# Kernel optimization log

Measured on AMD Instinct MI355X. Metric: run time of the kernel, lower is better.

## Reference

```python
import jax, jax.numpy as jnp
import numpy as np
import math


def setup_inputs() -> dict:
    key = jax.random.key(0)
    B, L, S, H, E = 16, 1024, 1024, 8, 64
    d = H * E  # d_model = 512
    ks = jax.random.split(key, 4)
    q = jax.random.normal(ks[0], (B, L, H, E), jnp.float32)
    k = jax.random.normal(ks[1], (B, S, H, E), jnp.float32)
    v = jax.random.normal(ks[2], (B, S, H, E), jnp.float32)
    # Conv1d(d_model, 2*d_model, kernel_size=3) weights [out, in, kw]
    W = jax.random.normal(ks[3], (2 * d, d, 3), jnp.float32) * (1.0 / math.sqrt(3 * d))
    b = jnp.zeros((2 * d,), jnp.float32)
    mask = jnp.zeros((B, L, S), jnp.bool_)  # unused by the module
    return {"q": q, "k": k, "v": v, "W": W, "b": b, "mask": mask}


def _fourier_attention(q, k, v, W, b):
    B, L, H, E = q.shape
    d = H * E
    # freq_enhance: Conv1d(d, 2d, k=3, pad=1) + GLU over channel dim
    x = q.reshape(B, L, d).transpose(0, 2, 1)  # [B, d, L]
    y = jax.lax.conv_general_dilated(
        x, W, window_strides=(1,), padding=[(1, 1)],
        dimension_numbers=("NCH", "OIH", "NCH"),
    ) + b[None, :, None]  # [B, 2d, L]
    a, g = jnp.split(y, 2, axis=1)
    q2 = (a * jax.nn.sigmoid(g)).transpose(0, 2, 1).reshape(B, L, H, E)

    xq = q2.transpose(0, 2, 3, 1)  # [B,H,E,L]
    xk = k.transpose(0, 2, 3, 1)   # [B,H,E,S]
    xv = v.transpose(0, 2, 3, 1)   # [B,H,E,S]

    qf = jnp.fft.rfft(xq, axis=-1, norm="ortho")  # [B,H,E,Lf]
    kf = jnp.fft.rfft(xk, axis=-1, norm="ortho")  # [B,H,E,Sf]
    vf = jnp.fft.rfft(xv, axis=-1, norm="ortho")  # [B,H,E,Sf]

    # complex cross-frequency scores [B,H,Lf,Sf]
    s = jnp.einsum("bhex,bhey->bhxy", qf, jnp.conj(kf)) / math.sqrt(E)

    # 'softmax' branch: magnitude gating + L1 normalization, keep phase
    mag = jnp.abs(s)
    phase = jnp.angle(s)
    mag = mag * (1.0 + jax.nn.sigmoid(mag))
    attn = mag / jnp.maximum(jnp.sum(mag, axis=-1, keepdims=True), 1e-12)  # F.normalize p=1
    sc = attn * jnp.exp(1j * phase)

    of = jnp.einsum("bhxy,bhey->bhex", sc, vf)  # [B,H,E,Lf]
    out = jnp.fft.irfft(of, n=L, axis=-1, norm="ortho").transpose(0, 3, 1, 2)  # [B,L,H,E]
    return out


def reference(q, k, v, W, b, mask):
    out = _fourier_attention(q, k, v, W, b)
    return out
```

## Files before the change

kernel.cpp:

```cpp
#include <hip/hip_runtime.h>
#include <math.h>


typedef __attribute__((ext_vector_type(8))) short bf16x8;
typedef __attribute__((ext_vector_type(4))) float f32x4;

union U8 { bf16x8 v; unsigned u[4]; };

__device__ __forceinline__ unsigned short f2b(float x) {
  unsigned u = __float_as_uint(x);
  return (unsigned short)((u + 0x7FFFu + ((u >> 16) & 1u)) >> 16);
}
__device__ __forceinline__ float b2f(unsigned short h) {
  return __uint_as_float(((unsigned)h) << 16);
}
__device__ __forceinline__ unsigned cvtpk_bf16(float lo, float hi) {
  unsigned r;
  asm("v_cvt_pk_bf16_f32 %0, %1, %2" : "=v"(r) : "v"(lo), "v"(hi));
  return r;
}

__device__ __forceinline__ void fft1024(float2* b0, float2* b1,
                                        const float2* twd, int tid) {
  float2* src = b0;
  float2* dst = b1;
#pragma unroll
  for (int st = 0; st < 10; ++st) {
    __syncthreads();
#pragma unroll
    for (int qq = 0; qq < 2; ++qq) {
      int bi = tid + qq * 256;
      int m = 1 << st;
      int j = bi >> st;
      int jm = j << st;
      float2 c0 = src[bi];
      float2 c1 = src[bi + 512];
      float2 w = twd[jm];
      float2 sum, dif, tw;
      sum.x = c0.x + c1.x; sum.y = c0.y + c1.y;
      dif.x = c0.x - c1.x; dif.y = c0.y - c1.y;
      tw.x = dif.x * w.x - dif.y * w.y;
      tw.y = dif.x * w.y + dif.y * w.x;
      dst[bi + jm] = sum;
      dst[bi + jm + m] = tw;
    }
    float2* tmp = src; src = dst; dst = tmp;
  }
  __syncthreads();
}

__global__ __launch_bounds__(256) void transpose_kernel(
    const float* __restrict__ in, float* __restrict__ out) {
  __shared__ float tile[32][33];
  int b = blockIdx.z;
  int s0 = blockIdx.x * 32;
  int c0 = blockIdx.y * 32;
  int tx = threadIdx.x & 31;
  int ty = threadIdx.x >> 5;
  const float* ip = in + (size_t)b * (1024 * 512);
  float* op = out + (size_t)b * (1024 * 512);
#pragma unroll
  for (int i = 0; i < 32; i += 8)
    tile[ty + i][tx] = ip[(size_t)(s0 + ty + i) * 512 + c0 + tx];
  __syncthreads();
#pragma unroll
  for (int i = 0; i < 32; i += 8)
    op[(size_t)(c0 + ty + i) * 1024 + s0 + tx] = tile[tx][ty + i];
}

__global__ __launch_bounds__(256) void transpose_q_split(
    const float* __restrict__ in, unsigned* __restrict__ XPhi,
    unsigned* __restrict__ XPlo) {
  __shared__ float tile[32][33];
  int b = blockIdx.z;
  int l0 = blockIdx.x * 32;
  int c0 = blockIdx.y * 32;
  int tx = threadIdx.x & 31;
  int ty = threadIdx.x >> 5;
  const float* ip = in + (size_t)b * (1024 * 512);
#pragma unroll
  for (int i = 0; i < 32; i += 8)
    tile[ty + i][tx] = ip[(size_t)(l0 + ty + i) * 512 + c0 + tx];
  __syncthreads();
  int p = threadIdx.x & 15;
  int lb = threadIdx.x >> 4;
#pragma unroll
  for (int i = 0; i < 2; ++i) {
    int ll = lb + i * 16;
    float v0 = tile[ll][2 * p];
    float v1 = tile[ll][2 * p + 1];
    unsigned short h0 = f2b(v0), h1 = f2b(v1);
    unsigned short q0 = f2b(v0 - b2f(h0)), q1 = f2b(v1 - b2f(h1));
    size_t o = ((size_t)b * 1024 + l0 + ll) * 256 + (c0 >> 1) + p;
    XPhi[o] = (unsigned)h0 | ((unsigned)h1 << 16);
    XPlo[o] = (unsigned)q0 | ((unsigned)q1 << 16);
  }
}

__global__ __launch_bounds__(256) void transpose_w_split(
    const float* __restrict__ Win, uint2* __restrict__ Wsp) {
  __shared__ float tile[32][49];
  int og0 = blockIdx.x * 32;
  int ct0 = blockIdx.y * 48;
  int tid = threadIdx.x;
#pragma unroll
  for (int i = 0; i < 6; ++i) {
    int flat = tid + i * 256;
    int og = flat / 48, ct = flat % 48;
    tile[og][ct] = Win[(size_t)(og0 + og) * 1536 + ct0 + ct];
  }
  __syncthreads();
  int ogl = tid & 31;
  int s = tid >> 5;
#pragma unroll
  for (int i = 0; i < 3; ++i) {
    int pt = s + i * 8;
    int pl = pt / 3, t = pt % 3;
    float v0 = tile[ogl][pl * 6 + t];
    float v1 = tile[ogl][pl * 6 + 3 + t];
    unsigned short h0 = f2b(v0), h1 = f2b(v1);
    unsigned short q0 = f2b(v0 - b2f(h0)), q1 = f2b(v1 - b2f(h1));
    Wsp[((size_t)(ct0 / 6 + pl) * 3 + t) * 1024 + og0 + ogl] =
        make_uint2((unsigned)h0 | ((unsigned)h1 << 16),
                   (unsigned)q0 | ((unsigned)q1 << 16));
  }
}

__global__ __launch_bounds__(256, 2) void conv_glu_mfma(
    const unsigned* __restrict__ XPhi, const unsigned* __restrict__ XPlo,
    const uint2* __restrict__ Wsp, const float* __restrict__ bias,
    float* __restrict__ q2t) {
  __shared__ unsigned Whi[3 * 64 * 18];
  __shared__ unsigned Wlo[3 * 64 * 18];

  int tid = threadIdx.x;
  int w = tid >> 6;
  int lane = tid & 63;
  int grp = lane >> 4;
  int lid = lane & 15;

  unsigned v0 = blockIdx.x;
  int xcd = (int)(v0 & 7u);
  int j = (int)(v0 >> 3);
  int b = xcd * 2 + (j >> 6);
  int rem = j & 63;
  int ca = (rem >> 2) * 32;
  int l0 = (rem & 3) * 256;

  const unsigned* xh = XPhi + (size_t)b * 1024 * 256;
  const unsigned* xl = XPlo + (size_t)b * 1024 * 256;

  f32x4 acc[4][4];
#pragma unroll
  for (int mi = 0; mi < 4; ++mi)
#pragma unroll
    for (int ni = 0; ni < 4; ++ni) acc[mi][ni] = {0.f, 0.f, 0.f, 0.f};

  for (int c0 = 0; c0 < 512; c0 += 32) {
    __syncthreads();
#pragma unroll
    for (int i = 0; i < 12; ++i) {
      int flat = tid + i * 256;
      int ogi = flat & 63;
      int r = flat >> 6;
      int t = r % 3, p = r / 3;
      int og = (ogi < 32) ? (ca + ogi) : (480 + ca + ogi);
      uint2 g = Wsp[((size_t)((c0 >> 1) + p) * 3 + t) * 1024 + og];
      Whi[(t * 64 + ogi) * 18 + p] = g.x;
      Wlo[(t * 64 + ogi) * 18 + p] = g.y;
    }
    __syncthreads();

#pragma unroll
    for (int t = 0; t < 3; ++t) {
      U8 Ah[4], Al[4];
#pragma unroll
      for (int mi = 0; mi < 4; ++mi) {
        int base = (t * 64 + mi * 16 + lid) * 18 + 4 * grp;
        uint2 h0 = *(const uint2*)&Whi[base];
        uint2 h1 = *(const uint2*)&Whi[base + 2];
        uint2 g0 = *(const uint2*)&Wlo[base];
        uint2 g1 = *(const uint2*)&Wlo[base + 2];
        Ah[mi].u[0] = h0.x; Ah[mi].u[1] = h0.y;
        Ah[mi].u[2] = h1.x; Ah[mi].u[3] = h1.y;
        Al[mi].u[0] = g0.x; Al[mi].u[1] = g0.y;
        Al[mi].u[2] = g1.x; Al[mi].u[3] = g1.y;
      }
      U8 Bh[4], Bl[4];
#pragma unroll
      for (int ni = 0; ni < 4; ++ni) {
        unsigned gl = (unsigned)(l0 + w * 64 + ni * 16 + lid + t - 1);
        uint4 dh = make_uint4(0, 0, 0, 0), dl = make_uint4(0, 0, 0, 0);
        if (gl < 1024u) {
          size_t off = (size_t)gl * 256 + (c0 >> 1) + 4 * grp;
          dh = *(const uint4*)(xh + off);
          dl = *(const uint4*)(xl + off);
        }
        Bh[ni].u[0] = dh.x; Bh[ni].u[1] = dh.y;
        Bh[ni].u[2] = dh.z; Bh[ni].u[3] = dh.w;
        Bl[ni].u[0] = dl.x; Bl[ni].u[1] = dl.y;
        Bl[ni].u[2] = dl.z; Bl[ni].u[3] = dl.w;
      }
#pragma unroll
      for (int mi = 0; mi < 4; ++mi)
#pragma unroll
        for (int ni = 0; ni < 4; ++ni) {
          acc[mi][ni] = __builtin_amdgcn_mfma_f32_16x16x32_bf16(
              Ah[mi].v, Bl[ni].v, acc[mi][ni], 0, 0, 0);
          acc[mi][ni] = __builtin_amdgcn_mfma_f32_16x16x32_bf16(
              Al[mi].v, Bh[ni].v, acc[mi][ni], 0, 0, 0);
          acc[mi][ni] = __builtin_amdgcn_mfma_f32_16x16x32_bf16(
              Ah[mi].v, Bh[ni].v, acc[mi][ni], 0, 0, 0);
        }
    }
  }

#pragma unroll
  for (int mi = 0; mi < 2; ++mi)
#pragma unroll
    for (int rr = 0; rr < 4; ++rr) {
      int row = mi * 16 + grp * 4 + rr;
      float ba = bias[ca + row];
      float bg = bias[512 + ca + row];
      float* orow =
          q2t + ((size_t)b * 512 + ca + row) * 1024 + l0 + w * 64 + lid;
#pragma unroll
      for (int ni = 0; ni < 4; ++ni) {
        float a = acc[mi][ni][rr] + ba;
        float g = acc[mi + 2][ni][rr] + bg;
        orow[ni * 16] = a / (1.f + __expf(-g));
      }
    }
}

__global__ __launch_bounds__(256) void fft_fwd_kernel(
    const float* __restrict__ in, ushort4* __restrict__ out, float scale) {
  __shared__ float2 sb0[1024];
  __shared__ float2 sb1[1024];
  __shared__ float2 twd[512];
  int tid = threadIdx.x;
  size_t r = blockIdx.x;
  const float* ip = in + r * 1024;
#pragma unroll
  for (int i = 0; i < 4; ++i) {
    int idx = tid + i * 256;
    sb0[idx] = make_float2(ip[idx], 0.f);
  }
  for (int kk = tid; kk < 512; kk += 256) {
    float ang = -6.283185307179586f * (float)kk * (1.0f / 1024.0f);
    float sn, cs;
    __sincosf(ang, &sn, &cs);
    twd[kk] = make_float2(cs, sn);
  }
  fft1024(sb0, sb1, twd, tid);
  ushort4* op = out + r * 514;
  for (int x = tid; x < 513; x += 256) {
    float2 v = sb0[x];
    float re = v.x * scale, im = v.y * scale;
    unsigned short rh = f2b(re), ih = f2b(im);
    unsigned short rl = f2b(re - b2f(rh)), il = f2b(im - b2f(ih));
    op[x] = make_ushort4(rh, ih, rl, il);
  }
  if (tid == 0) op[513] = make_ushort4(0, 0, 0, 0);
}

__global__ __launch_bounds__(256) void vft_kernel(
    const uint2* __restrict__ vf, uint2* __restrict__ vfT) {
  __shared__ uint2 tile[64][65];
  int bh = blockIdx.y;
  int y0 = blockIdx.x * 64;
  int tid = threadIdx.x;
  const uint2* src = vf + (size_t)bh * 64 * 514;
  uint2* dst = vfT + (size_t)bh * 514 * 64;
#pragma unroll
  for (int i = 0; i < 16; ++i) {
    int flat = tid + i * 256;
    int e = flat >> 6, y = flat & 63;
    int gy = y0 + y;
    uint2 d = make_uint2(0, 0);
    if (gy < 514) d = src[(size_t)e * 514 + gy];
    tile[e][y] = d;
  }
  __syncthreads();
#pragma unroll
  for (int i = 0; i < 16; ++i) {
    int flat = tid + i * 256;
    int y = flat >> 6, e = flat & 63;
    int gy = y0 + y;
    if (gy < 514) dst[(size_t)gy * 64 + e] = tile[e][y];
  }
}

template <bool TAIL>
__device__ __forceinline__ void attn_tile(
    int y0, const uint2* __restrict__ kb, const uint2* __restrict__ vb,
    const U8 (&Ah)[2][4], const U8 (&Al)[2][4],
    unsigned* Shi, unsigned* Slo, float* zacc, f32x4* ore, f32x4* oim,
    int w, int grp, int lid) {
  int yk = y0 + 16 * w + lid;
  uint2 BK[4][4];
  bool kval = !TAIL || (yk < 514);
#pragma unroll
  for (int ks = 0; ks < 4; ++ks)
#pragma unroll
    for (int jp = 0; jp < 4; ++jp) {
      int e = ks * 16 + grp * 4 + jp;
      if (!TAIL) {
        BK[ks][jp] = kb[(size_t)e * 514 + yk];
      } else {
        uint2 d = make_uint2(0, 0);
        if (kval) d = kb[(size_t)e * 514 + yk];
        BK[ks][jp] = d;
      }
    }
  f32x4 cre[2] = {{0.f, 0.f, 0.f, 0.f}, {0.f, 0.f, 0.f, 0.f}};
  f32x4 cim[2] = {{0.f, 0.f, 0.f, 0.f}, {0.f, 0.f, 0.f, 0.f}};
#pragma unroll
  for (int ks = 0; ks < 4; ++ks) {
    U8 bhh, bll, bih, bil;
#pragma unroll
    for (int jp = 0; jp < 4; ++jp) {
      unsigned uh = BK[ks][jp].x, ul = BK[ks][jp].y;
      bhh.u[jp] = uh;
      bll.u[jp] = ul;
      bih.u[jp] = ((uh >> 16) ^ 0x8000u) | (uh << 16);
      bil.u[jp] = ((ul >> 16) ^ 0x8000u) | (ul << 16);
    }
#pragma unroll
    for (int mt = 0; mt < 2; ++mt) {
      cre[mt] = __builtin_amdgcn_mfma_f32_16x16x32_bf16(Ah[mt][ks].v, bhh.v, cre[mt], 0, 0, 0);
      cre[mt] = __builtin_amdgcn_mfma_f32_16x16x32_bf16(Al[mt][ks].v, bhh.v, cre[mt], 0, 0, 0);
      cre[mt] = __builtin_amdgcn_mfma_f32_16x16x32_bf16(Ah[mt][ks].v, bll.v, cre[mt], 0, 0, 0);
      cim[mt] = __builtin_amdgcn_mfma_f32_16x16x32_bf16(Ah[mt][ks].v, bih.v, cim[mt], 0, 0, 0);
      cim[mt] = __builtin_amdgcn_mfma_f32_16x16x32_bf16(Al[mt][ks].v, bih.v, cim[mt], 0, 0, 0);
      cim[mt] = __builtin_amdgcn_mfma_f32_16x16x32_bf16(Ah[mt][ks].v, bil.v, cim[mt], 0, 0, 0);
    }
  }
#pragma unroll
  for (int mt = 0; mt < 2; ++mt)
#pragma unroll
    for (int r = 0; r < 4; ++r) {
      float sre = cre[mt][r], sim = cim[mt][r];
      float m = sqrtf(sre * sre + sim * sim);
      float f = 1.f + 1.f / (1.f + __expf(-m));
      zacc[mt * 4 + r] += m * f;
      float wre = sre * f, wim = sim * f;
      unsigned dh = cvtpk_bf16(wre, wim);
      float rre = wre - __uint_as_float(dh << 16);
      float rim = wim - __uint_as_float(dh & 0xffff0000u);
      unsigned dl = cvtpk_bf16(rre, rim);
      int x = mt * 16 + grp * 4 + r;
      int idx = x * 64 + ((16 * w + lid) ^ ((x & 15) << 2));
      Shi[idx] = dh;
      Slo[idx] = dl;
    }
  __syncthreads();
#pragma unroll
  for (int ks = 0; ks < 4; ++ks) {
    uint2 BV[4];
#pragma unroll
    for (int jp = 0; jp < 4; ++jp) {
      int yv = y0 + ks * 16 + grp * 4 + jp;
      if (!TAIL) {
        BV[jp] = vb[(size_t)yv * 64 + 16 * w + lid];
      } else {
        uint2 d = make_uint2(0, 0);
        if (yv < 514) d = vb[(size_t)yv * 64 + 16 * w + lid];
        BV[jp] = d;
      }
    }
    U8 bvh, bvl, bvi, bvj;
#pragma unroll
    for (int jp = 0; jp < 4; ++jp) {
      unsigned uh = BV[jp].x, ul = BV[jp].y;
      bvh.u[jp] = uh ^ 0x80000000u;
      bvl.u[jp] = ul ^ 0x80000000u;
      bvi.u[jp] = (uh >> 16) | (uh << 16);
      bvj.u[jp] = (ul >> 16) | (ul << 16);
    }
#pragma unroll
    for (int mt = 0; mt < 2; ++mt) {
      int sidx = (mt * 16 + lid) * 64 + ((ks * 16 + grp * 4) ^ (lid << 2));
      U8 a2h, a2l;
      a2h.v = *(const bf16x8*)&Shi[sidx];
      a2l.v = *(const bf16x8*)&Slo[sidx];
      ore[mt] = __builtin_amdgcn_mfma_f32_16x16x32_bf16(a2h.v, bvh.v, ore[mt], 0, 0, 0);
      ore[mt] = __builtin_amdgcn_mfma_f32_16x16x32_bf16(a2l.v, bvh.v, ore[mt], 0, 0, 0);
      ore[mt] = __builtin_amdgcn_mfma_f32_16x16x32_bf16(a2h.v, bvl.v, ore[mt], 0, 0, 0);
      oim[mt] = __builtin_amdgcn_mfma_f32_16x16x32_bf16(a2h.v, bvi.v, oim[mt], 0, 0, 0);
      oim[mt] = __builtin_amdgcn_mfma_f32_16x16x32_bf16(a2l.v, bvi.v, oim[mt], 0, 0, 0);
      oim[mt] = __builtin_amdgcn_mfma_f32_16x16x32_bf16(a2h.v, bvj.v, oim[mt], 0, 0, 0);
    }
  }
  __syncthreads();
}

__global__ __launch_bounds__(256, 3) void attn_kernel(
    const uint2* __restrict__ qf, const uint2* __restrict__ kf,
    const uint2* __restrict__ vfT, float2* __restrict__ of) {
  __shared__ __align__(16) unsigned char smem[16896];
  unsigned* Shi = (unsigned*)smem;
  unsigned* Slo = (unsigned*)(smem + 8192);
  float* zred = (float*)(smem + 16384);

  int tid = threadIdx.x;
  int w = tid >> 6;
  int lane = tid & 63;
  int grp = lane >> 4;
  int lid = lane & 15;

  unsigned v0 = blockIdx.x;
  unsigned cc = v0 & 7u;
  unsigned jj = v0 >> 3;
  int bh = (int)(cc + 8u * (jj / 17u));
  int x0 = (int)(jj % 17u) * 32;

  const uint2* qb = qf + (size_t)bh * (64 * 514);
  const uint2* kb = kf + (size_t)bh * (64 * 514);
  const uint2* vb = vfT + (size_t)bh * (514 * 64);

  U8 Ah[2][4], Al[2][4];
#pragma unroll
  for (int mt = 0; mt < 2; ++mt) {
    int gx = x0 + mt * 16 + lid;
    bool qv = gx < 514;
#pragma unroll
    for (int ks = 0; ks < 4; ++ks)
#pragma unroll
      for (int jp = 0; jp < 4; ++jp) {
        int e = ks * 16 + grp * 4 + jp;
        uint2 d = make_uint2(0, 0);
        if (qv) d = qb[(size_t)e * 514 + gx];
        Ah[mt][ks].u[jp] = d.x;
        Al[mt][ks].u[jp] = d.y;
      }
  }

  float zacc[8] = {0.f, 0.f, 0.f, 0.f, 0.f, 0.f, 0.f, 0.f};
  f32x4 ore[2] = {{0.f, 0.f, 0.f, 0.f}, {0.f, 0.f, 0.f, 0.f}};
  f32x4 oim[2] = {{0.f, 0.f, 0.f, 0.f}, {0.f, 0.f, 0.f, 0.f}};

#pragma unroll 1
  for (int yt = 0; yt < 8; ++yt)
    attn_tile<false>(yt * 64, kb, vb, Ah, Al, Shi, Slo, zacc, ore, oim,
                     w, grp, lid);
  attn_tile<true>(512, kb, vb, Ah, Al, Shi, Slo, zacc, ore, oim,
                  w, grp, lid);

#pragma unroll
  for (int mt = 0; mt < 2; ++mt)
#pragma unroll
    for (int r = 0; r < 4; ++r) {
      float z = zacc[mt * 4 + r];
      z += __shfl_xor(z, 1); z += __shfl_xor(z, 2);
      z += __shfl_xor(z, 4); z += __shfl_xor(z, 8);
      zacc[mt * 4 + r] = z;
    }
  if (lid == 0) {
#pragma unroll
    for (int mt = 0; mt < 2; ++mt)
#pragma unroll
      for (int r = 0; r < 4; ++r)
        zred[w * 32 + mt * 16 + grp * 4 + r] = zacc[mt * 4 + r];
  }
  __syncthreads();
  float2* ov = (float2*)smem;
#pragma unroll
  for (int mt = 0; mt < 2; ++mt)
#pragma unroll
    for (int r = 0; r < 4; ++r) {
      int x = mt * 16 + grp * 4 + r;
      float z = zred[x] + zred[32 + x] + zred[64 + x] + zred[96 + x];
      float inv = 1.f / fmaxf(z, 1e-12f);
      int e = w * 16 + lid;
      ov[e * 32 + (x ^ ((e & 7) << 2))] =
          make_float2(ore[mt][r] * inv, oim[mt][r] * inv);
    }
  __syncthreads();
  {
    float2* ob = of + (size_t)bh * 64 * 513;
#pragma unroll
    for (int i = 0; i < 4; ++i) {
      int e = (tid >> 4) + i * 16;
      int xq = (tid & 15) * 2;
      int sw = (e & 7) << 2;
      float2 a = ov[e * 32 + (xq ^ sw)];
      float2 b2 = ov[e * 32 + ((xq + 1) ^ sw)];
      int gx = x0 + xq;
      if (gx < 513) ob[(size_t)e * 513 + gx] = a;
      if (gx + 1 < 513) ob[(size_t)e * 513 + gx + 1] = b2;
    }
  }
}

__global__ __launch_bounds__(256) void fft_inv_kernel(
    const float2* __restrict__ in, float* __restrict__ out) {
  __shared__ float2 sb0[1024];
  __shared__ float2 sb1[1024];
  __shared__ float2 twd[512];
  int tid = threadIdx.x;
  size_t r = blockIdx.x;
  const float2* ip = in + r * 513;
#pragma unroll
  for (int i = 0; i < 4; ++i) {
    int idx = tid + i * 256;
    float2 v;
    if (idx < 513) {
      v = ip[idx];
    } else {
      float2 u = ip[1024 - idx];
      v = make_float2(u.x, -u.y);
    }
    sb0[idx] = v;
  }
  for (int kk = tid; kk < 512; kk += 256) {
    float ang = 6.283185307179586f * (float)kk * (1.0f / 1024.0f);
    float sn, cs;
    __sincosf(ang, &sn, &cs);
    twd[kk] = make_float2(cs, sn);
  }
  fft1024(sb0, sb1, twd, tid);
  int e = (int)(r & 63);
  int h = (int)((r >> 6) & 7);
  size_t b = r >> 9;
  float* op = out + b * (size_t)(1024 * 512) + (size_t)h * 64 + e;
  const float sc = 0.03125f;
#pragma unroll
  for (int i = 0; i < 4; ++i) {
    int l = tid + i * 256;
    op[(size_t)l * 512] = sb0[l].x * sc;
  }
}

extern "C" void kernel_launch(void* const* d_in, const int* in_sizes, int n_in,
                              void* d_out, int out_size, void* d_ws, size_t ws_size,
                              hipStream_t stream) {
  const float* q = (const float*)d_in[0];
  const float* k = (const float*)d_in[1];
  const float* v = (const float*)d_in[2];
  const float* W = (const float*)d_in[3];
  const float* bias = (const float*)d_in[4];
  float* out = (float*)d_out;

  float* wsf = (float*)d_ws;
  float*    A    = wsf;
  uint2*    vfT  = (uint2*)wsf;
  unsigned* XPhi = (unsigned*)(wsf + 8421376);
  unsigned* XPlo = XPhi + (size_t)16 * 1024 * 256;
  ushort4*  qf   = (ushort4*)(wsf + 8421376);
  uint2*    Wsp  = (uint2*)(wsf + 16842752);
  ushort4*  vf   = (ushort4*)(wsf + 16842752);
  float2*   of   = (float2*)(wsf + 16842752);
  ushort4*  kf   = (ushort4*)(wsf + 25264128);

  transpose_q_split<<<dim3(32, 16, 16), 256, 0, stream>>>(q, XPhi, XPlo);
  transpose_w_split<<<dim3(32, 32), 256, 0, stream>>>(W, Wsp);
  conv_glu_mfma<<<dim3(1024), 256, 0, stream>>>(XPhi, XPlo, Wsp, bias, A);
  fft_fwd_kernel<<<dim3(8192), 256, 0, stream>>>(A, qf, 0.03125f * 0.125f);
  transpose_kernel<<<dim3(32, 16, 16), 256, 0, stream>>>(k, A);
  fft_fwd_kernel<<<dim3(8192), 256, 0, stream>>>(A, kf, 0.03125f);
  transpose_kernel<<<dim3(32, 16, 16), 256, 0, stream>>>(v, A);
  fft_fwd_kernel<<<dim3(8192), 256, 0, stream>>>(A, vf, 0.03125f);
  vft_kernel<<<dim3(9, 128), 256, 0, stream>>>((const uint2*)vf, vfT);
  attn_kernel<<<dim3(2176), 256, 0, stream>>>((const uint2*)qf, (const uint2*)kf,
                                              vfT, of);
  fft_inv_kernel<<<dim3(8192), 256, 0, stream>>>(of, out);
}
```

Baseline: 774.3 us.

## Double-buffer conv weights in LDS and prefetch activation tiles in registers

The conv+GLU MFMA kernel now double-buffers the weight tile in shared memory. The next chunk's weights are loaded into registers mid-iteration and written to the alternate buffer, so only one barrier is needed per iteration. Activation B-fragments for the next tap or channel chunk are prefetched into registers while the current MFMAs run, to hide global load latency. This raises register pressure and LDS use, which could hurt occupancy under the 2-block launch bound.

```diff
diff --git a/kernel.cpp b/kernel.cpp
--- a/kernel.cpp
+++ b/kernel.cpp
@@ -130,8 +130,8 @@
     const unsigned* __restrict__ XPhi, const unsigned* __restrict__ XPlo,
     const uint2* __restrict__ Wsp, const float* __restrict__ bias,
     float* __restrict__ q2t) {
-  __shared__ unsigned Whi[3 * 64 * 18];
-  __shared__ unsigned Wlo[3 * 64 * 18];
+  __shared__ unsigned Whi[2][3 * 64 * 18];
+  __shared__ unsigned Wlo[2][3 * 64 * 18];
 
   int tid = threadIdx.x;
   int w = tid >> 6;
@@ -150,69 +150,115 @@
   const unsigned* xh = XPhi + (size_t)b * 1024 * 256;
   const unsigned* xl = XPlo + (size_t)b * 1024 * 256;
 
+  int lbase = l0 + w * 64 + lid;
+
   f32x4 acc[4][4];
 #pragma unroll
   for (int mi = 0; mi < 4; ++mi)
 #pragma unroll
     for (int ni = 0; ni < 4; ++ni) acc[mi][ni] = {0.f, 0.f, 0.f, 0.f};
 
+  uint4 Bh_c[4], Bl_c[4];
+  uint4 Bh_n[4], Bl_n[4];
+
+#pragma unroll
+  for (int ni = 0; ni < 4; ++ni) {
+    int gl = lbase + ni * 16 - 1;
+    uint4 dh = make_uint4(0, 0, 0, 0), dl = make_uint4(0, 0, 0, 0);
+    if ((unsigned)gl < 1024u) {
+      size_t off = (size_t)gl * 256 + 4 * grp;
+      dh = *(const uint4*)(xh + off);
+      dl = *(const uint4*)(xl + off);
+    }
+    Bh_c[ni] = dh; Bl_c[ni] = dl;
+  }
+#pragma unroll
+  for (int i = 0; i < 12; ++i) {
+    int flat = tid + i * 256;
+    int ogi = flat & 63;
+    int r = flat >> 6;
+    int tt = r % 3, p = r / 3;
+    int og = (ogi < 32) ? (ca + ogi) : (480 + ca + ogi);
+    uint2 g = Wsp[((size_t)p * 3 + tt) * 1024 + og];
+    Whi[0][(tt * 64 + ogi) * 18 + p] = g.x;
+    Wlo[0][(tt * 64 + ogi) * 18 + p] = g.y;
+  }
+  __syncthreads();
+
+#pragma unroll 1
   for (int c0 = 0; c0 < 512; c0 += 32) {
-    __syncthreads();
+    int cur = (c0 >> 5) & 1;
+    int cnp = ((c0 + 32) & 511) >> 1;
+    uint2 wreg[12];
+
+#pragma unroll
+    for (int t = 0; t < 3; ++t) {
+      int cpn = (t < 2) ? (c0 >> 1) : cnp;
+      int tn = (t < 2) ? (t + 1) : 0;
+#pragma unroll
+      for (int ni = 0; ni < 4; ++ni) {
+        int gl = lbase + ni * 16 + tn - 1;
+        uint4 dh = make_uint4(0, 0, 0, 0), dl = make_uint4(0, 0, 0, 0);
+        if ((unsigned)gl < 1024u) {
+          size_t off = (size_t)gl * 256 + cpn + 4 * grp;
+          dh = *(const uint4*)(xh + off);
+          dl = *(const uint4*)(xl + off);
+        }
+        Bh_n[ni] = dh; Bl_n[ni] = dl;
+      }
+      if (t == 1) {
+#pragma unroll
+        for (int i = 0; i < 12; ++i) {
+          int flat = tid + i * 256;
+          int ogi = flat & 63;
+          int r = flat >> 6;
+          int tt = r % 3, p = r / 3;
+          int og = (ogi < 32) ? (ca + ogi) : (480 + ca + ogi);
+          wreg[i] = Wsp[((size_t)(cnp + p) * 3 + tt) * 1024 + og];
+        }
+      }
+#pragma unroll
+      for (int mi = 0; mi < 4; ++mi) {
+        U8 Ah, Al;
+        {
+          int base = (t * 64 + mi * 16 + lid) * 18 + 4 * grp;
+          uint2 h0 = *(const uint2*)&Whi[cur][base];
+          uint2 h1 = *(const uint2*)&Whi[cur][base + 2];
+          uint2 g0 = *(const uint2*)&Wlo[cur][base];
+          uint2 g1 = *(const uint2*)&Wlo[cur][base + 2];
+          Ah.u[0] = h0.x; Ah.u[1] = h0.y; Ah.u[2] = h1.x; Ah.u[3] = h1.y;
+          Al.u[0] = g0.x; Al.u[1] = g0.y; Al.u[2] = g1.x; Al.u[3] = g1.y;
+        }
+#pragma unroll
+        for (int ni = 0; ni < 4; ++ni) {
+          U8 Bh, Bl;
+          Bh.u[0] = Bh_c[ni].x; Bh.u[1] = Bh_c[ni].y;
+          Bh.u[2] = Bh_c[ni].z; Bh.u[3] = Bh_c[ni].w;
+          Bl.u[0] = Bl_c[ni].x; Bl.u[1] = Bl_c[ni].y;
+          Bl.u[2] = Bl_c[ni].z; Bl.u[3] = Bl_c[ni].w;
+          acc[mi][ni] = __builtin_amdgcn_mfma_f32_16x16x32_bf16(
+              Ah.v, Bl.v, acc[mi][ni], 0, 0, 0);
+          acc[mi][ni] = __builtin_amdgcn_mfma_f32_16x16x32_bf16(
+              Al.v, Bh.v, acc[mi][ni], 0, 0, 0);
+          acc[mi][ni] = __builtin_amdgcn_mfma_f32_16x16x32_bf16(
+              Ah.v, Bh.v, acc[mi][ni], 0, 0, 0);
+        }
+      }
+#pragma unroll
+      for (int ni = 0; ni < 4; ++ni) {
+        Bh_c[ni] = Bh_n[ni]; Bl_c[ni] = Bl_n[ni];
+      }
+    }
 #pragma unroll
     for (int i = 0; i < 12; ++i) {
       int flat = tid + i * 256;
       int ogi = flat & 63;
       int r = flat >> 6;
-      int t = r % 3, p = r / 3;
-      int og = (ogi < 32) ? (ca + ogi) : (480 + ca + ogi);
-      uint2 g = Wsp[((size_t)((c0 >> 1) + p) * 3 + t) * 1024 + og];
-      Whi[(t * 64 + ogi) * 18 + p] = g.x;
-      Wlo[(t * 64 + ogi) * 18 + p] = g.y;
+      int tt = r % 3, p = r / 3;
+      Whi[cur ^ 1][(tt * 64 + ogi) * 18 + p] = wreg[i].x;
+      Wlo[cur ^ 1][(tt * 64 + ogi) * 18 + p] = wreg[i].y;
     }
     __syncthreads();
-
-#pragma unroll
-    for (int t = 0; t < 3; ++t) {
-      U8 Ah[4], Al[4];
-#pragma unroll
-      for (int mi = 0; mi < 4; ++mi) {
-        int base = (t * 64 + mi * 16 + lid) * 18 + 4 * grp;
-        uint2 h0 = *(const uint2*)&Whi[base];
-        uint2 h1 = *(const uint2*)&Whi[base + 2];
-        uint2 g0 = *(const uint2*)&Wlo[base];
-        uint2 g1 = *(const uint2*)&Wlo[base + 2];
-        Ah[mi].u[0] = h0.x; Ah[mi].u[1] = h0.y;
-        Ah[mi].u[2] = h1.x; Ah[mi].u[3] = h1.y;
-        Al[mi].u[0] = g0.x; Al[mi].u[1] = g0.y;
-        Al[mi].u[2] = g1.x; Al[mi].u[3] = g1.y;
-      }
-      U8 Bh[4], Bl[4];
-#pragma unroll
-      for (int ni = 0; ni < 4; ++ni) {
-        unsigned gl = (unsigned)(l0 + w * 64 + ni * 16 + lid + t - 1);
-        uint4 dh = make_uint4(0, 0, 0, 0), dl = make_uint4(0, 0, 0, 0);
-        if (gl < 1024u) {
-          size_t off = (size_t)gl * 256 + (c0 >> 1) + 4 * grp;
-          dh = *(const uint4*)(xh + off);
-          dl = *(const uint4*)(xl + off);
-        }
-        Bh[ni].u[0] = dh.x; Bh[ni].u[1] = dh.y;
-        Bh[ni].u[2] = dh.z; Bh[ni].u[3] = dh.w;
-        Bl[ni].u[0] = dl.x; Bl[ni].u[1] = dl.y;
-        Bl[ni].u[2] = dl.z; Bl[ni].u[3] = dl.w;
-      }
-#pragma unroll
-      for (int mi = 0; mi < 4; ++mi)
-#pragma unroll
-        for (int ni = 0; ni < 4; ++ni) {
-          acc[mi][ni] = __builtin_amdgcn_mfma_f32_16x16x32_bf16(
-              Ah[mi].v, Bl[ni].v, acc[mi][ni], 0, 0, 0);
-          acc[mi][ni] = __builtin_amdgcn_mfma_f32_16x16x32_bf16(
-              Al[mi].v, Bh[ni].v, acc[mi][ni], 0, 0, 0);
-          acc[mi][ni] = __builtin_amdgcn_mfma_f32_16x16x32_bf16(
-              Ah[mi].v, Bh[ni].v, acc[mi][ni], 0, 0, 0);
-        }
-    }
   }
 
 #pragma unroll
```

Measured after the change: 811.6 us. 4.8% more time.
